# Kernel optimization log

Measured on AMD Instinct MI355X. Metric: run time of the kernel, lower is better.

Reference implementation:

```python
import jax, jax.numpy as jnp
import numpy as np

B, N, ND_, FEAT, WV = 32, 1024, 8, 2048, 300
E, T, STEPS = 20000, 2, 5
NDIM = N * ND_  # 8192


def setup_inputs() -> dict:
    key = jax.random.key(0)
    ks = jax.random.split(key, 20)
    s = 0.02
    inputs = jax.random.normal(ks[0], (B, FEAT), jnp.float32)
    wordvecs = jax.random.normal(ks[1], (N, WV), jnp.float32)
    # unique edges per type (disjoint across types) so the scatter has no duplicate indices
    rng = np.random.default_rng(0)
    codes = rng.permutation(N * N)[: T * E].reshape(T, E)
    edge_u = (codes // N).astype(np.int32)
    edge_v = (codes % N).astype(np.int32)
    ki = np.repeat(np.arange(ND_), ND_)
    kj = np.tile(np.arange(ND_), ND_)
    mat_u = (edge_u.reshape(-1)[:, None] * ND_ + ki[None, :]).reshape(-1).astype(np.int32)
    mat_v = (edge_v.reshape(-1)[:, None] * ND_ + kj[None, :]).reshape(-1).astype(np.int32)
    p = {
        'inputs': inputs, 'wordvecs': wordvecs,
        'edge_u': jnp.asarray(edge_u), 'edge_v': jnp.asarray(edge_v),
        'mat_u': jnp.asarray(mat_u), 'mat_v': jnp.asarray(mat_v),
        # Inputnet: Linear(feat+wv -> 512), Linear(512 -> node_dim)
        'W_in1': jax.random.normal(ks[2], (512, FEAT + WV), jnp.float32) * s,
        'b_in1': jnp.zeros((512,), jnp.float32),
        'W_in2': jax.random.normal(ks[3], (ND_, 512), jnp.float32) * s,
        'b_in2': jnp.zeros((ND_,), jnp.float32),
        # embnet: Linear(wv -> 50)
        'W_emb': jax.random.normal(ks[4], (50, WV), jnp.float32) * s,
        'b_emb': jnp.zeros((50,), jnp.float32),
        # relnets: one (50, 50*nd^2) matrix per edge type
        'rel_mats': jax.random.normal(ks[5], (T, 50, 50 * ND_ * ND_), jnp.float32) * s,
        # GRUCell(node_dim, node_dim)
        'W_ih': jax.random.normal(ks[6], (3 * ND_, ND_), jnp.float32) * s,
        'W_hh': jax.random.normal(ks[7], (3 * ND_, ND_), jnp.float32) * s,
        'b_ih': jnp.zeros((3 * ND_,), jnp.float32),
        'b_hh': jnp.zeros((3 * ND_,), jnp.float32),
        # outnet: Linear(nd -> 20), ReLU, Linear(20 -> 1)
        'W_o1': jax.random.normal(ks[8], (20, ND_), jnp.float32) * s,
        'b_o1': jnp.zeros((20,), jnp.float32),
        'W_o2': jax.random.normal(ks[9], (1, 20), jnp.float32) * s,
        'b_o2': jnp.zeros((1,), jnp.float32),
    }
    return p


def reference(inputs, wordvecs, edge_u, edge_v, mat_u, mat_v,
              W_in1, b_in1, W_in2, b_in2, W_emb, b_emb, rel_mats,
              W_ih, W_hh, b_ih, b_hh, W_o1, b_o1, W_o2, b_o2):
    nd = W_in2.shape[0]
    n_nodes = wordvecs.shape[0]
    ndim = n_nodes * nd
    bsz = inputs.shape[0]

    # Inputnet: per-(image, node) feature -> initial hidden state [B, N*nd]
    f = jnp.concatenate([
        jnp.broadcast_to(inputs[:, None, :], (bsz, n_nodes, inputs.shape[1])),
        jnp.broadcast_to(wordvecs[None, :, :], (bsz, n_nodes, wordvecs.shape[1])),
    ], axis=-1).reshape(bsz * n_nodes, -1)
    h = jax.nn.relu(f @ W_in1.T + b_in1) @ W_in2.T + b_in2  # [B*N, nd]
    hidden = h.reshape(bsz, ndim)

    # edge weights via Relnet per edge type
    embs = wordvecs @ W_emb.T + b_emb  # [N, 50]
    ws = []
    for t in range(rel_mats.shape[0]):
        ue = embs[edge_u[t]]  # [E, 50]
        ve = embs[edge_v[t]]  # [E, 50]
        tmp = (ue @ rel_mats[t]).reshape(ue.shape[0], embs.shape[1], nd * nd)
        ws.append(jnp.einsum('ed,edk->ek', ve, tmp))  # [E, nd^2]
    weights = jnp.concatenate(ws, axis=0).reshape(-1)

    # scatter into dense propagation matrix
    P = jnp.zeros((ndim, ndim), jnp.float32).at[mat_u, mat_v].set(weights)
    norm = jnp.sqrt(jnp.sum(P * P, axis=1))  # row L2 norms [ndim]
    norm = norm + (norm == 0).astype(P.dtype)
    P = P / norm  # NOTE: torch broadcasting divides COLUMNS by row norms (faithful)

    def gru(x, hc):
        gi = x @ W_ih.T + b_ih
        gh = hc @ W_hh.T + b_hh
        ir, iz, inn = jnp.split(gi, 3, axis=-1)
        hr, hz, hn = jnp.split(gh, 3, axis=-1)
        r = jax.nn.sigmoid(ir + hr)
        z = jax.nn.sigmoid(iz + hz)
        n = jnp.tanh(inn + r * hn)
        return (1.0 - z) * n + z * hc

    hiddens = [hidden]
    for _ in range(STEPS):
        x = jnp.tanh(hidden @ P.T)  # [B, ndim]
        hidden = gru(x.reshape(-1, nd), hidden.reshape(-1, nd)).reshape(bsz, ndim)
        hiddens.append(hidden)
    states = jnp.stack(hiddens, axis=1)  # [B, STEPS+1, ndim]

    o = jax.nn.relu(states.reshape(-1, nd) @ W_o1.T + b_o1) @ W_o2.T + b_o2  # [B*(S+1)*N, 1]
    logits = o.reshape(bsz, STEPS + 1, n_nodes).transpose(0, 2, 1)  # [B, N, S+1]
    return logits
```

## Files before the change

### kernel.cpp

```cpp
#include <hip/hip_runtime.h>
#include <math.h>

constexpr int B = 32, N = 1024, ND = 8, FEAT = 2048, WVD = 300;
constexpr int E = 20000, T = 2, STEPS = 5;
constexpr int NDIM = N * ND;
constexpr int H1 = 512;
constexpr int W1C = FEAT + WVD;
constexpr int EMB = 50;
constexpr int RC = EMB * ND * ND;
constexpr int SEG = 16;
constexpr int SEGLEN = E / SEG;
constexpr int KH = 150;

constexpr int G_KA   = 512;
constexpr int G_W1T  = 16 * 10;
constexpr int G_EMB  = N * 25 / 4;
constexpr int G_SEGH = T * N * SEG / 4;
constexpr int F1_TOT = G_KA + G_W1T + G_EMB + G_SEGH;

constexpr int G_ARED = 8;
constexpr int G_WV2  = 512;
constexpr int G_AHAT = 13 * (N / 32) * T;
constexpr int F2_TOT = 1 + G_ARED + G_WV2 + G_AHAT;

constexpr int F4_TOT = 2 * N;

__global__ __launch_bounds__(256) void k_f1(
        const int* eu, int* segcnt,
        const float* inp, const float* W1, float* partA, float* W1T,
        const float* wv, const float* We, const float* be,
        float* embs, float* embsT) {
    __shared__ float smem[8 * 260];
    int tid = threadIdx.x;
    int blk = blockIdx.x;
    if (blk < G_KA) {
        int c = tid & 7, b = tid >> 3;
        int c0 = (blk & 63) * 8;
        int ks = blk >> 6;
        int kt = ks * 256;
        {
            int r = tid >> 5, cb = (tid & 31) * 8;
            const float* src = W1 + (size_t)(c0 + r) * W1C + kt + cb;
            float4 a0 = *(const float4*)src;
            float4 a1 = *(const float4*)(src + 4);
            *(float4*)&smem[r * 260 + cb] = a0;
            *(float4*)&smem[r * 260 + cb + 4] = a1;
        }
        __syncthreads();
        const float* xr = inp + (size_t)b * FEAT + kt;
        float acc = 0.f;
#pragma unroll 8
        for (int k4 = 0; k4 < 64; k4++) {
            float4 x = *(const float4*)(xr + k4 * 4);
            float4 w = *(const float4*)&smem[c * 260 + k4 * 4];
            acc += x.x * w.x + x.y * w.y + x.z * w.z + x.w * w.w;
        }
        partA[(size_t)ks * (H1 * B) + (c0 + c) * B + b] = acc;
    } else if (blk < G_KA + G_W1T) {
        int lb = blk - G_KA;
        int c0 = (lb % 16) * 32, k0 = (lb / 16) * 32;
        float (*tile)[33] = (float(*)[33])smem;
        int kl = tid & 31, cl4 = tid >> 5;
#pragma unroll
        for (int p = 0; p < 4; p++) {
            int c = cl4 + p * 8;
            int k = k0 + kl;
            if (k < WVD) tile[c][kl] = W1[(size_t)(c0 + c) * W1C + FEAT + k];
        }
        __syncthreads();
        int cl = tid & 31, kl4 = tid >> 5;
#pragma unroll
        for (int p = 0; p < 4; p++) {
            int kk = kl4 + p * 8;
            int k = k0 + kk;
            if (k < WVD) W1T[(size_t)k * H1 + c0 + cl] = tile[cl][kk];
        }
    } else if (blk < G_KA + G_W1T + G_EMB) {
        int lb = blk - G_KA - G_W1T;
        int wid = lb * 4 + (tid >> 6);
        int lane = tid & 63;
        int n = wid / 25, cp = wid - n * 25;
        int c0 = cp * 2;
        const float* xr = wv + (size_t)n * WVD;
        const float* wr0 = We + (size_t)c0 * WVD;
        const float* wr1 = wr0 + WVD;
        float a0 = 0.f, a1 = 0.f;
#pragma unroll
        for (int i = 0; i < 5; i++) {
            int k = i * 64 + lane;
            if (k < WVD) {
                float x = xr[k];
                a0 += x * wr0[k];
                a1 += x * wr1[k];
            }
        }
        for (int m = 32; m; m >>= 1) {
            a0 += __shfl_xor(a0, m, 64);
            a1 += __shfl_xor(a1, m, 64);
        }
        if (lane == 0) {
            float v0 = a0 + be[c0], v1 = a1 + be[c0 + 1];
            embs[n * EMB + c0] = v0;
            embs[n * EMB + c0 + 1] = v1;
            embsT[c0 * N + n] = v0;
            embsT[(c0 + 1) * N + n] = v1;
        }
    } else {
        int lb = blk - G_KA - G_W1T - G_EMB;
        int wid = lb * 4 + (tid >> 6);
        int lane = tid & 63;
        int t = wid >> 14, u = (wid >> 4) & (N - 1), seg = wid & (SEG - 1);
        const int* eut = eu + t * E;
        int e0 = seg * SEGLEN, e1 = e0 + SEGLEN, cnt = 0;
        for (int c = e0; c < e1; c += 64) {
            int e = c + lane;
            bool ok = (e < e1) && (eut[e] == u);
            cnt += __popcll(__ballot(ok));
        }
        if (lane == 0) segcnt[wid] = cnt;
    }
}

__global__ __launch_bounds__(256) void k_f2(
        const int* segcnt, int* segoff, int* counts, int* ptr,
        const float* partA, float* AbT,
        const float* wv, const float* W1T, float* Wp,
        const float* embsT, const float* RMbase, float* Ahat) {
    __shared__ float smemf[4096];
    int tid = threadIdx.x, blk = blockIdx.x;
    if (blk == 0) {
        int* sc = (int*)smemf;
        for (int row = tid; row < 2048; row += 256) {
            int acc = 0;
            const int* src = segcnt + row * SEG;
            int* dst = segoff + row * SEG;
#pragma unroll
            for (int s = 0; s < SEG; s++) { dst[s] = acc; acc += src[s]; }
            counts[row] = acc;
            sc[row] = acc;
        }
        __syncthreads();
        int* src = sc; int* dst = sc + 2048;
        for (int st = 1; st < 2048; st <<= 1) {
            for (int j = tid; j < 2048; j += 256)
                dst[j] = src[j] + (j >= st ? src[j - st] : 0);
            __syncthreads();
            int* tmp = src; src = dst; dst = tmp;
        }
        for (int j = tid; j < 2048; j += 256)
            ptr[j] = j ? src[j - 1] : 0;
    } else if (blk <= G_ARED) {
        int cb = (blk - 1) * 2048 + tid * 8;
        if (cb < H1 * B) {
            float4 s0 = {0, 0, 0, 0}, s1 = {0, 0, 0, 0};
#pragma unroll
            for (int ks = 0; ks < 8; ks++) {
                const float* p = partA + (size_t)ks * (H1 * B) + cb;
                float4 a = *(const float4*)p;
                float4 b4 = *(const float4*)(p + 4);
                s0.x += a.x; s0.y += a.y; s0.z += a.z; s0.w += a.w;
                s1.x += b4.x; s1.y += b4.y; s1.z += b4.z; s1.w += b4.w;
            }
            *(float4*)(AbT + cb) = s0;
            *(float4*)(AbT + cb + 4) = s1;
        }
    } else if (blk <= G_ARED + G_WV2) {
        int lb = blk - 1 - G_ARED;
        int kh = lb >> 8;
        int rem = lb & 255;
        int c = (rem & 1) * 256 + tid;
        int n0 = (rem >> 1) * 8;
        int kb = kh * KH;
        float (*el)[152] = (float(*)[152])smemf;
        for (int idx = tid; idx < 8 * KH; idx += 256) {
            int j = idx / KH, k = idx - j * KH;
            el[j][k] = wv[(size_t)(n0 + j) * WVD + kb + k];
        }
        __syncthreads();
        float acc[8] = {};
#pragma unroll 5
        for (int k = 0; k < KH; k++) {
            float r = W1T[(size_t)(kb + k) * H1 + c];
#pragma unroll
            for (int j = 0; j < 8; j++) acc[j] += el[j][k] * r;
        }
        float* wout = Wp + (size_t)kh * N * H1;
#pragma unroll
        for (int j = 0; j < 8; j++) wout[(size_t)(n0 + j) * H1 + c] = acc[j];
    } else {
        int lb = blk - 1 - G_ARED - G_WV2;
        int t = lb / (13 * 32), r = lb % (13 * 32);
        int bx = r % 13, by = r / 13;
        const float* RM = RMbase + (size_t)t * EMB * RC;
        float* Ah = Ahat + (size_t)t * N * RC;
        int n0 = by * 32;
        float (*el)[36] = (float(*)[36])smemf;
        for (int idx = tid; idx < EMB * 32; idx += 256)
            el[idx >> 5][idx & 31] = embsT[(idx >> 5) * N + n0 + (idx & 31)];
        __syncthreads();
        int mi = bx * 256 + (tid & 63) * 4;
        int ni = (tid >> 6) * 8;
        if (mi < RC) {
            float acc[8][4] = {};
#pragma unroll 2
            for (int c = 0; c < EMB; c++) {
                float4 rm = *(const float4*)(RM + (size_t)c * RC + mi);
                float4 e0 = *(const float4*)&el[c][ni];
                float4 e1 = *(const float4*)&el[c][ni + 4];
                float ev[8] = {e0.x, e0.y, e0.z, e0.w, e1.x, e1.y, e1.z, e1.w};
#pragma unroll
                for (int j = 0; j < 8; j++) {
                    acc[j][0] += ev[j] * rm.x;
                    acc[j][1] += ev[j] * rm.y;
                    acc[j][2] += ev[j] * rm.z;
                    acc[j][3] += ev[j] * rm.w;
                }
            }
#pragma unroll
            for (int j = 0; j < 8; j++) {
                float4 o = {acc[j][0], acc[j][1], acc[j][2], acc[j][3]};
                *(float4*)(Ah + (size_t)(n0 + ni + j) * RC + mi) = o;
            }
        }
    }
}

__global__ __launch_bounds__(256) void k_f3(
        const int* eu, const int* ev, const int* ptr, const int* segoff, int* sv) {
    int tid = threadIdx.x, blk = blockIdx.x;
    int wid = blk * 4 + (tid >> 6);
    int lane = tid & 63;
    int t = wid >> 14, u = (wid >> 4) & (N - 1), seg = wid & (SEG - 1);
    const int* eut = eu + t * E;
    const int* evt = ev + t * E;
    int row = t * N + u;
    int base = ptr[row] + segoff[row * SEG + seg];
    int e0 = seg * SEGLEN, e1 = e0 + SEGLEN, cnt = 0;
    for (int c = e0; c < e1; c += 64) {
        int e = c + lane;
        bool ok = (e < e1) && (eut[e] == u);
        unsigned long long m = __ballot(ok);
        if (ok) {
            int rank = __popcll(m & ((1ull << lane) - 1));
            sv[base + cnt + rank] = evt[e];
        }
        cnt += __popcll(m);
    }
}

__global__ __launch_bounds__(256) void k_f4(
        const int* ptr, const int* counts, const int* sv,
        const float* embs, const float* Ahat, float* wbuf, float* inorm,
        const float* AbT, const float* Wp, const float* b1,
        const float* W2, const float* b2, float* sT0) {
    __shared__ float smem[6656];
    int tid = threadIdx.x;
    int blk = blockIdx.x;
    if (blk < N) {
        float* AL = smem;
        int u = blk;
        int wv_ = tid >> 6, k = tid & 63;
        float ssq = 0.f;
        for (int t = 0; t < T; t++) {
            __syncthreads();
            for (int idx = tid; idx < RC; idx += 256)
                AL[idx] = Ahat[((size_t)t * N + u) * RC + idx];
            __syncthreads();
            int base = ptr[t * N + u], cnt = counts[t * N + u];
            for (int i = wv_; i < cnt; i += 4) {
                int slot = base + i;
                int v = sv[slot];
                const float* vr = embs + v * EMB;
                float acc = 0.f;
#pragma unroll 10
                for (int d = 0; d < EMB; d++) acc += vr[d] * AL[d * 64 + k];
                wbuf[(size_t)slot * 64 + k] = acc;
                ssq += acc * acc;
            }
        }
        __syncthreads();
        AL[wv_ * 64 + k] = ssq;
        __syncthreads();
        if (tid < 64) {
            float tot = AL[tid] + AL[64 + tid] + AL[128 + tid] + AL[192 + tid];
            tot += __shfl_xor(tot, 1, 64);
            tot += __shfl_xor(tot, 2, 64);
            tot += __shfl_xor(tot, 4, 64);
            int ki = tid >> 3, kj = tid & 7;
            if (kj == 0) {
                float nv = sqrtf(tot);
                if (nv == 0.f) nv = 1.f;
                inorm[u * ND + ki] = 1.0f / nv;
            }
        }
    } else {
        int n = blk - N;
        float* w2s  = smem;
        float* wvs  = smem + 4096;
        float* part = smem + 4608;
        for (int idx = tid; idx < 8 * H1; idx += 256) w2s[idx] = W2[idx];
        for (int idx = tid; idx < H1; idx += 256)
            wvs[idx] = Wp[(size_t)n * H1 + idx]
                     + Wp[(size_t)N * H1 + (size_t)n * H1 + idx] + b1[idx];
        __syncthreads();
        int b = tid & 31, s = tid >> 5;
        float acc[8] = {};
        for (int i = 0; i < 64; i++) {
            int c = s * 64 + i;
            float tv = fmaxf(AbT[c * 32 + b] + wvs[c], 0.f);
#pragma unroll
            for (int ki = 0; ki < 8; ki++) acc[ki] += tv * w2s[ki * H1 + c];
        }
#pragma unroll
        for (int ki = 0; ki < 8; ki++) part[s * 256 + ki * 32 + b] = acc[ki];
        __syncthreads();
        int ki2 = tid >> 5, b2i = tid & 31;
        float tot = b2[ki2];
#pragma unroll
        for (int s2 = 0; s2 < 8; s2++) tot += part[s2 * 256 + ki2 * 32 + b2i];
        sT0[(size_t)n * 256 + tid] = tot;
    }
}

__global__ __launch_bounds__(256) void k_sc(const int* sv, float* wbuf,
                                            const float* inorm) {
    int idx = blockIdx.x * 256 + threadIdx.x;
    int slot = idx >> 6, k = idx & 63;
    int v = sv[slot];
    wbuf[idx] = wbuf[idx] * inorm[v * ND + (k & 7)];
}

__global__ __launch_bounds__(256) void k_step(
        const int* ptr, const int* counts, const int* sv,
        const float* wbuf, const float* sT, int s,
        const float* W_ih, const float* W_hh, const float* b_ih, const float* b_hh,
        const float* Wo1, const float* bo1, const float* Wo2, const float* bo2,
        float* sOut, float* out, int last) {
    __shared__ float xs[256], hs[256], hfin[256];
    __shared__ float wih[192], whh[192];
    __shared__ float w1s[160], b1s[20], w2s[20];
    __shared__ float res[8][33];
    int tid = threadIdx.x;
    int u = blockIdx.x;
    int ki = tid >> 5, b = tid & 31;
    if (tid < 192) { wih[tid] = W_ih[tid]; whh[tid] = W_hh[tid]; }
    if (last) {
        if (tid < 160) w1s[tid] = Wo1[tid];
        if (tid < 20) { b1s[tid] = bo1[tid]; w2s[tid] = Wo2[tid]; }
    }
    const float* sIn = sT + (size_t)s * NDIM * B;
    float hown = sIn[((size_t)u * 8 + ki) * B + b];
    float acc = 0.f;
    for (int t = 0; t < T; t++) {
        int base = ptr[t * N + u], cnt = counts[t * N + u];
        int i = 0;
        for (; i + 1 < cnt; i += 2) {
            int s0 = base + i, s1 = base + i + 1;
            int v0 = sv[s0], v1 = sv[s1];
            const float* wp0 = wbuf + (size_t)s0 * 64 + ki * 8;
            const float* wp1 = wbuf + (size_t)s1 * 64 + ki * 8;
            float4 wa0 = *(const float4*)wp0;
            float4 wb0 = *(const float4*)(wp0 + 4);
            float4 wa1 = *(const float4*)wp1;
            float4 wb1 = *(const float4*)(wp1 + 4);
            const float* hp0 = sIn + (size_t)v0 * 256 + b;
            const float* hp1 = sIn + (size_t)v1 * 256 + b;
            acc += wa0.x * hp0[0]   + wa0.y * hp0[32]  + wa0.z * hp0[64]  + wa0.w * hp0[96]
                 + wb0.x * hp0[128] + wb0.y * hp0[160] + wb0.z * hp0[192] + wb0.w * hp0[224];
            acc += wa1.x * hp1[0]   + wa1.y * hp1[32]  + wa1.z * hp1[64]  + wa1.w * hp1[96]
                 + wb1.x * hp1[128] + wb1.y * hp1[160] + wb1.z * hp1[192] + wb1.w * hp1[224];
        }
        if (i < cnt) {
            int s0 = base + i;
            int v0 = sv[s0];
            const float* wp0 = wbuf + (size_t)s0 * 64 + ki * 8;
            float4 wa0 = *(const float4*)wp0;
            float4 wb0 = *(const float4*)(wp0 + 4);
            const float* hp0 = sIn + (size_t)v0 * 256 + b;
            acc += wa0.x * hp0[0]   + wa0.y * hp0[32]  + wa0.z * hp0[64]  + wa0.w * hp0[96]
                 + wb0.x * hp0[128] + wb0.y * hp0[160] + wb0.z * hp0[192] + wb0.w * hp0[224];
        }
    }
    float xv = tanhf(acc);
    xs[ki * 32 + b] = xv;
    hs[ki * 32 + b] = hown;
    __syncthreads();
    float gr = b_ih[ki], gz = b_ih[8 + ki], gn = b_ih[16 + ki];
    float hr = b_hh[ki], hz = b_hh[8 + ki], hn = b_hh[16 + ki];
#pragma unroll
    for (int j = 0; j < 8; j++) {
        float xj = xs[j * 32 + b], hj = hs[j * 32 + b];
        gr += wih[ki * 8 + j] * xj;
        gz += wih[(8 + ki) * 8 + j] * xj;
        gn += wih[(16 + ki) * 8 + j] * xj;
        hr += whh[ki * 8 + j] * hj;
        hz += whh[(8 + ki) * 8 + j] * hj;
        hn += whh[(16 + ki) * 8 + j] * hj;
    }
    float r = 1.f / (1.f + expf(-(gr + hr)));
    float z = 1.f / (1.f + expf(-(gz + hz)));
    float nn = tanhf(gn + r * hn);
    float hnew = (1.f - z) * nn + z * hown;
    if (!last) {
        sOut[((size_t)u * 8 + ki) * B + b] = hnew;
        return;
    }
    hfin[ki * 32 + b] = hnew;
    __syncthreads();
    int s6 = tid >> 5, bb = tid & 31;
    if (s6 < 6) {
        float x[8];
#pragma unroll
        for (int kk = 0; kk < 8; kk++)
            x[kk] = (s6 < STEPS)
                ? sT[((size_t)s6 * NDIM + u * 8 + kk) * B + bb]
                : hfin[kk * 32 + bb];
        float accv = bo2[0];
#pragma unroll
        for (int j = 0; j < 20; j++) {
            float h = b1s[j];
#pragma unroll
            for (int kk = 0; kk < 8; kk++) h += w1s[j * 8 + kk] * x[kk];
            h = fmaxf(h, 0.f);
            accv += w2s[j] * h;
        }
        res[s6][bb] = accv;
    }
    __syncthreads();
    if (tid < 192) {
        int b_w = tid / 6, s_w = tid - b_w * 6;
        out[(size_t)b_w * ((STEPS + 1) * N) + u * (STEPS + 1) + s_w] = res[s_w][b_w];
    }
}

extern "C" void kernel_launch(void* const* d_in, const int* in_sizes, int n_in,
                              void* d_out, int out_size, void* d_ws, size_t ws_size,
                              hipStream_t stream) {
    const float* inputs   = (const float*)d_in[0];
    const float* wordvecs = (const float*)d_in[1];
    const int*   edge_u   = (const int*)d_in[2];
    const int*   edge_v   = (const int*)d_in[3];
    const float* W_in1 = (const float*)d_in[6];
    const float* b_in1 = (const float*)d_in[7];
    const float* W_in2 = (const float*)d_in[8];
    const float* b_in2 = (const float*)d_in[9];
    const float* W_emb = (const float*)d_in[10];
    const float* b_emb = (const float*)d_in[11];
    const float* rel_mats = (const float*)d_in[12];
    const float* W_ih = (const float*)d_in[13];
    const float* W_hh = (const float*)d_in[14];
    const float* b_ih = (const float*)d_in[15];
    const float* b_hh = (const float*)d_in[16];
    const float* W_o1 = (const float*)d_in[17];
    const float* b_o1 = (const float*)d_in[18];
    const float* W_o2 = (const float*)d_in[19];
    const float* b_o2 = (const float*)d_in[20];
    float* out = (float*)d_out;

    char* ws = (char*)d_ws;
    size_t off = 0;
    auto alloc = [&](size_t bytes) -> void* {
        void* p = ws + off;
        off = (off + bytes + 255) & ~(size_t)255;
        return p;
    };
    int* segcnt    = (int*)alloc((size_t)T * N * SEG * 4);
    int* segoff    = (int*)alloc((size_t)T * N * SEG * 4);
    int* counts    = (int*)alloc(2048 * 4);
    int* ptr       = (int*)alloc(2048 * 4);
    int* sv        = (int*)alloc((size_t)T * E * 4);
    float* inorm   = (float*)alloc((size_t)NDIM * 4);
    float* partA   = (float*)alloc((size_t)8 * H1 * B * 4);
    float* AbT     = (float*)alloc((size_t)H1 * B * 4);
    float* W1T     = (float*)alloc((size_t)WVD * H1 * 4);
    float* Wp      = (float*)alloc((size_t)2 * N * H1 * 4);
    float* embs    = (float*)alloc((size_t)N * EMB * 4);
    float* embsT   = (float*)alloc((size_t)EMB * N * 4);
    float* Ahat    = (float*)alloc((size_t)T * N * RC * 4);
    float* wbuf    = (float*)alloc((size_t)T * E * 64 * 4);
    float* sT      = (float*)alloc((size_t)(STEPS + 1) * NDIM * B * 4);

    k_f1<<<F1_TOT, 256, 0, stream>>>(edge_u, segcnt, inputs, W_in1, partA, W1T,
                                     wordvecs, W_emb, b_emb, embs, embsT);
    k_f2<<<F2_TOT, 256, 0, stream>>>(segcnt, segoff, counts, ptr,
                                     partA, AbT,
                                     wordvecs, W1T, Wp, embsT, rel_mats, Ahat);
    k_f3<<<T * N * SEG / 4, 256, 0, stream>>>(edge_u, edge_v, ptr, segoff, sv);
    k_f4<<<F4_TOT, 256, 0, stream>>>(ptr, counts, sv, embs, Ahat, wbuf, inorm,
                                     AbT, Wp, b_in1, W_in2, b_in2, sT);
    k_sc<<<T * E * 64 / 256, 256, 0, stream>>>(sv, wbuf, inorm);

    for (int s = 0; s < STEPS; s++) {
        int last = (s == STEPS - 1) ? 1 : 0;
        k_step<<<N, 256, 0, stream>>>(ptr, counts, sv, wbuf, sT, s,
                                      W_ih, W_hh, b_ih, b_hh,
                                      W_o1, b_o1, W_o2, b_o2,
                                      sT + (size_t)(s + 1) * NDIM * B, out, last);
    }
}
```

Measured before the change: 276.0 us.

## Fuse edge bucketing into per-node weight kernel; fold norm scaling into step

Replaces the segmented count, prefix-scan and scatter passes that built a CSR edge list with a per-node scan inside the weight kernel. Each block collects its own node's neighbours through wave ballots into fixed-capacity (64) slots. The separate column-norm rescale kernel is dropped and inorm is applied on the fly inside each propagation step. This cuts three launches and one full pass over wbuf. In exchange, every node block now scans all edges of both types, each step does extra inorm loads, and correctness depends on no node having more than 64 edges per type.

```diff
diff --git a/kernel.cpp b/kernel.cpp
--- a/kernel.cpp
+++ b/kernel.cpp
@@ -8,25 +8,21 @@
 constexpr int W1C = FEAT + WVD;
 constexpr int EMB = 50;
 constexpr int RC = EMB * ND * ND;
-constexpr int SEG = 16;
-constexpr int SEGLEN = E / SEG;
 constexpr int KH = 150;
+constexpr int CAP = 64;
+constexpr int EQ = E / 4;
 
 constexpr int G_KA   = 512;
 constexpr int G_W1T  = 16 * 10;
 constexpr int G_EMB  = N * 25 / 4;
-constexpr int G_SEGH = T * N * SEG / 4;
-constexpr int F1_TOT = G_KA + G_W1T + G_EMB + G_SEGH;
+constexpr int F1_TOT = G_KA + G_W1T + G_EMB;
 
 constexpr int G_ARED = 8;
-constexpr int G_WV2  = 512;
-constexpr int G_AHAT = 13 * (N / 32) * T;
-constexpr int F2_TOT = 1 + G_ARED + G_WV2 + G_AHAT;
-
-constexpr int F4_TOT = 2 * N;
+constexpr int G_WV   = 512;
+constexpr int G_AHAT = 13 * 32 * T;
+constexpr int F2_TOT = G_ARED + G_WV + G_AHAT;
 
 __global__ __launch_bounds__(256) void k_f1(
-        const int* eu, int* segcnt,
         const float* inp, const float* W1, float* partA, float* W1T,
         const float* wv, const float* We, const float* be,
         float* embs, float* embsT) {
@@ -75,7 +71,7 @@
             int k = k0 + kk;
             if (k < WVD) W1T[(size_t)k * H1 + c0 + cl] = tile[cl][kk];
         }
-    } else if (blk < G_KA + G_W1T + G_EMB) {
+    } else {
         int lb = blk - G_KA - G_W1T;
         int wid = lb * 4 + (tid >> 6);
         int lane = tid & 63;
@@ -105,91 +101,58 @@
             embsT[c0 * N + n] = v0;
             embsT[(c0 + 1) * N + n] = v1;
         }
-    } else {
-        int lb = blk - G_KA - G_W1T - G_EMB;
-        int wid = lb * 4 + (tid >> 6);
-        int lane = tid & 63;
-        int t = wid >> 14, u = (wid >> 4) & (N - 1), seg = wid & (SEG - 1);
-        const int* eut = eu + t * E;
-        int e0 = seg * SEGLEN, e1 = e0 + SEGLEN, cnt = 0;
-        for (int c = e0; c < e1; c += 64) {
-            int e = c + lane;
-            bool ok = (e < e1) && (eut[e] == u);
-            cnt += __popcll(__ballot(ok));
-        }
-        if (lane == 0) segcnt[wid] = cnt;
     }
 }
 
 __global__ __launch_bounds__(256) void k_f2(
-        const int* segcnt, int* segoff, int* counts, int* ptr,
         const float* partA, float* AbT,
         const float* wv, const float* W1T, float* Wp,
         const float* embsT, const float* RMbase, float* Ahat) {
-    __shared__ float smemf[4096];
+    __shared__ float smemf[1800];
     int tid = threadIdx.x, blk = blockIdx.x;
-    if (blk == 0) {
-        int* sc = (int*)smemf;
-        for (int row = tid; row < 2048; row += 256) {
-            int acc = 0;
-            const int* src = segcnt + row * SEG;
-            int* dst = segoff + row * SEG;
-#pragma unroll
-            for (int s = 0; s < SEG; s++) { dst[s] = acc; acc += src[s]; }
-            counts[row] = acc;
-            sc[row] = acc;
-        }
-        __syncthreads();
-        int* src = sc; int* dst = sc + 2048;
-        for (int st = 1; st < 2048; st <<= 1) {
-            for (int j = tid; j < 2048; j += 256)
-                dst[j] = src[j] + (j >= st ? src[j - st] : 0);
-            __syncthreads();
-            int* tmp = src; src = dst; dst = tmp;
-        }
-        for (int j = tid; j < 2048; j += 256)
-            ptr[j] = j ? src[j - 1] : 0;
-    } else if (blk <= G_ARED) {
-        int cb = (blk - 1) * 2048 + tid * 8;
-        if (cb < H1 * B) {
-            float4 s0 = {0, 0, 0, 0}, s1 = {0, 0, 0, 0};
-#pragma unroll
-            for (int ks = 0; ks < 8; ks++) {
-                const float* p = partA + (size_t)ks * (H1 * B) + cb;
-                float4 a = *(const float4*)p;
-                float4 b4 = *(const float4*)(p + 4);
-                s0.x += a.x; s0.y += a.y; s0.z += a.z; s0.w += a.w;
-                s1.x += b4.x; s1.y += b4.y; s1.z += b4.z; s1.w += b4.w;
-            }
-            *(float4*)(AbT + cb) = s0;
-            *(float4*)(AbT + cb + 4) = s1;
-        }
-    } else if (blk <= G_ARED + G_WV2) {
-        int lb = blk - 1 - G_ARED;
+    if (blk < G_ARED) {
+        int cb = blk * 2048 + tid * 8;
+        float4 s0 = {0, 0, 0, 0}, s1 = {0, 0, 0, 0};
+#pragma unroll
+        for (int ks = 0; ks < 8; ks++) {
+            const float* p = partA + (size_t)ks * (H1 * B) + cb;
+            float4 a = *(const float4*)p;
+            float4 b4 = *(const float4*)(p + 4);
+            s0.x += a.x; s0.y += a.y; s0.z += a.z; s0.w += a.w;
+            s1.x += b4.x; s1.y += b4.y; s1.z += b4.z; s1.w += b4.w;
+        }
+        *(float4*)(AbT + cb) = s0;
+        *(float4*)(AbT + cb + 4) = s1;
+    } else if (blk < G_ARED + G_WV) {
+        int lb = blk - G_ARED;
         int kh = lb >> 8;
         int rem = lb & 255;
         int c = (rem & 1) * 256 + tid;
         int n0 = (rem >> 1) * 8;
         int kb = kh * KH;
-        float (*el)[152] = (float(*)[152])smemf;
+        float (*el)[8] = (float(*)[8])smemf;
         for (int idx = tid; idx < 8 * KH; idx += 256) {
             int j = idx / KH, k = idx - j * KH;
-            el[j][k] = wv[(size_t)(n0 + j) * WVD + kb + k];
+            el[k][j] = wv[(size_t)(n0 + j) * WVD + kb + k];
         }
         __syncthreads();
         float acc[8] = {};
 #pragma unroll 5
         for (int k = 0; k < KH; k++) {
             float r = W1T[(size_t)(kb + k) * H1 + c];
-#pragma unroll
-            for (int j = 0; j < 8; j++) acc[j] += el[j][k] * r;
+            float4 e0 = *(const float4*)&el[k][0];
+            float4 e1 = *(const float4*)&el[k][4];
+            acc[0] += e0.x * r; acc[1] += e0.y * r;
+            acc[2] += e0.z * r; acc[3] += e0.w * r;
+            acc[4] += e1.x * r; acc[5] += e1.y * r;
+            acc[6] += e1.z * r; acc[7] += e1.w * r;
         }
         float* wout = Wp + (size_t)kh * N * H1;
 #pragma unroll
         for (int j = 0; j < 8; j++) wout[(size_t)(n0 + j) * H1 + c] = acc[j];
     } else {
-        int lb = blk - 1 - G_ARED - G_WV2;
-        int t = lb / (13 * 32), r = lb % (13 * 32);
+        int lb = blk - G_ARED - G_WV;
+        int t = lb / 416, r = lb % 416;
         int bx = r % 13, by = r / 13;
         const float* RM = RMbase + (size_t)t * EMB * RC;
         float* Ah = Ahat + (size_t)t * N * RC;
@@ -226,60 +189,75 @@
 }
 
 __global__ __launch_bounds__(256) void k_f3(
-        const int* eu, const int* ev, const int* ptr, const int* segoff, int* sv) {
-    int tid = threadIdx.x, blk = blockIdx.x;
-    int wid = blk * 4 + (tid >> 6);
-    int lane = tid & 63;
-    int t = wid >> 14, u = (wid >> 4) & (N - 1), seg = wid & (SEG - 1);
-    const int* eut = eu + t * E;
-    const int* evt = ev + t * E;
-    int row = t * N + u;
-    int base = ptr[row] + segoff[row * SEG + seg];
-    int e0 = seg * SEGLEN, e1 = e0 + SEGLEN, cnt = 0;
-    for (int c = e0; c < e1; c += 64) {
-        int e = c + lane;
-        bool ok = (e < e1) && (eut[e] == u);
-        unsigned long long m = __ballot(ok);
-        if (ok) {
-            int rank = __popcll(m & ((1ull << lane) - 1));
-            sv[base + cnt + rank] = evt[e];
-        }
-        cnt += __popcll(m);
-    }
-}
-
-__global__ __launch_bounds__(256) void k_f4(
-        const int* ptr, const int* counts, const int* sv,
+        const int* eu, const int* ev,
         const float* embs, const float* Ahat, float* wbuf, float* inorm,
+        int* counts, int* sv,
         const float* AbT, const float* Wp, const float* b1,
         const float* W2, const float* b2, float* sT0) {
     __shared__ float smem[6656];
+    __shared__ int vl[T][CAP];
+    __shared__ int wcnt[T][4];
     int tid = threadIdx.x;
     int blk = blockIdx.x;
     if (blk < N) {
+        int u = blk;
+        int w = tid >> 6, lane = tid & 63;
+        int* tmpv = (int*)smem;
+        for (int t = 0; t < T; t++) {
+            const int* eut = eu + t * E;
+            const int* evt = ev + t * E;
+            int q0 = w * EQ, q1 = q0 + EQ;
+            int cw = 0;
+            for (int c = q0; c < q1; c += 64) {
+                int e = c + lane;
+                bool ok = (e < q1) && (eut[e] == u);
+                unsigned long long m = __ballot(ok);
+                if (ok) {
+                    int rank = __popcll(m & ((1ull << lane) - 1));
+                    tmpv[(t * 4 + w) * CAP + cw + rank] = evt[e];
+                }
+                cw += __popcll(m);
+            }
+            if (lane == 0) wcnt[t][w] = cw;
+        }
+        __syncthreads();
+        int cnts[T];
+        for (int t = 0; t < T; t++) {
+            int base_w = 0;
+            for (int j = 0; j < w; j++) base_w += wcnt[t][j];
+            int mycnt = wcnt[t][w];
+            int row = t * N + u;
+            for (int i = lane; i < mycnt; i += 64) {
+                int vv = tmpv[(t * 4 + w) * CAP + i];
+                vl[t][base_w + i] = vv;
+                sv[row * CAP + base_w + i] = vv;
+            }
+            cnts[t] = wcnt[t][0] + wcnt[t][1] + wcnt[t][2] + wcnt[t][3];
+            if (tid == 0) counts[row] = cnts[t];
+        }
+        __syncthreads();
         float* AL = smem;
-        int u = blk;
-        int wv_ = tid >> 6, k = tid & 63;
+        int k = lane;
         float ssq = 0.f;
         for (int t = 0; t < T; t++) {
             __syncthreads();
             for (int idx = tid; idx < RC; idx += 256)
                 AL[idx] = Ahat[((size_t)t * N + u) * RC + idx];
             __syncthreads();
-            int base = ptr[t * N + u], cnt = counts[t * N + u];
-            for (int i = wv_; i < cnt; i += 4) {
-                int slot = base + i;
-                int v = sv[slot];
+            int cnt = cnts[t];
+            size_t base = (size_t)(t * N + u) * CAP;
+            for (int i = w; i < cnt; i += 4) {
+                int v = vl[t][i];
                 const float* vr = embs + v * EMB;
                 float acc = 0.f;
 #pragma unroll 10
                 for (int d = 0; d < EMB; d++) acc += vr[d] * AL[d * 64 + k];
-                wbuf[(size_t)slot * 64 + k] = acc;
+                wbuf[(base + i) * 64 + k] = acc;
                 ssq += acc * acc;
             }
         }
         __syncthreads();
-        AL[wv_ * 64 + k] = ssq;
+        AL[w * 64 + k] = ssq;
         __syncthreads();
         if (tid < 64) {
             float tot = AL[tid] + AL[64 + tid] + AL[128 + tid] + AL[192 + tid];
@@ -322,17 +300,9 @@
     }
 }
 
-__global__ __launch_bounds__(256) void k_sc(const int* sv, float* wbuf,
-                                            const float* inorm) {
-    int idx = blockIdx.x * 256 + threadIdx.x;
-    int slot = idx >> 6, k = idx & 63;
-    int v = sv[slot];
-    wbuf[idx] = wbuf[idx] * inorm[v * ND + (k & 7)];
-}
-
 __global__ __launch_bounds__(256) void k_step(
-        const int* ptr, const int* counts, const int* sv,
-        const float* wbuf, const float* sT, int s,
+        const int* counts, const int* sv,
+        const float* wbuf, const float* inorm, const float* sT, int s,
         const float* W_ih, const float* W_hh, const float* b_ih, const float* b_hh,
         const float* Wo1, const float* bo1, const float* Wo2, const float* bo2,
         float* sOut, float* out, int last) {
@@ -352,33 +322,44 @@
     float hown = sIn[((size_t)u * 8 + ki) * B + b];
     float acc = 0.f;
     for (int t = 0; t < T; t++) {
-        int base = ptr[t * N + u], cnt = counts[t * N + u];
+        int row = t * N + u;
+        int cnt = counts[row];
+        size_t base = (size_t)row * CAP;
         int i = 0;
         for (; i + 1 < cnt; i += 2) {
-            int s0 = base + i, s1 = base + i + 1;
+            size_t s0 = base + i, s1 = base + i + 1;
             int v0 = sv[s0], v1 = sv[s1];
-            const float* wp0 = wbuf + (size_t)s0 * 64 + ki * 8;
-            const float* wp1 = wbuf + (size_t)s1 * 64 + ki * 8;
+            const float* wp0 = wbuf + s0 * 64 + ki * 8;
+            const float* wp1 = wbuf + s1 * 64 + ki * 8;
             float4 wa0 = *(const float4*)wp0;
             float4 wb0 = *(const float4*)(wp0 + 4);
             float4 wa1 = *(const float4*)wp1;
             float4 wb1 = *(const float4*)(wp1 + 4);
+            const float* ip0 = inorm + v0 * ND;
+            const float* ip1 = inorm + v1 * ND;
             const float* hp0 = sIn + (size_t)v0 * 256 + b;
             const float* hp1 = sIn + (size_t)v1 * 256 + b;
-            acc += wa0.x * hp0[0]   + wa0.y * hp0[32]  + wa0.z * hp0[64]  + wa0.w * hp0[96]
-                 + wb0.x * hp0[128] + wb0.y * hp0[160] + wb0.z * hp0[192] + wb0.w * hp0[224];
-            acc += wa1.x * hp1[0]   + wa1.y * hp1[32]  + wa1.z * hp1[64]  + wa1.w * hp1[96]
-                 + wb1.x * hp1[128] + wb1.y * hp1[160] + wb1.z * hp1[192] + wb1.w * hp1[224];
+            acc += (wa0.x * ip0[0]) * hp0[0]   + (wa0.y * ip0[1]) * hp0[32]
+                 + (wa0.z * ip0[2]) * hp0[64]  + (wa0.w * ip0[3]) * hp0[96]
+                 + (wb0.x * ip0[4]) * hp0[128] + (wb0.y * ip0[5]) * hp0[160]
+                 + (wb0.z * ip0[6]) * hp0[192] + (wb0.w * ip0[7]) * hp0[224];
+            acc += (wa1.x * ip1[0]) * hp1[0]   + (wa1.y * ip1[1]) * hp1[32]
+                 + (wa1.z * ip1[2]) * hp1[64]  + (wa1.w * ip1[3]) * hp1[96]
+                 + (wb1.x * ip1[4]) * hp1[128] + (wb1.y * ip1[5]) * hp1[160]
+                 + (wb1.z * ip1[6]) * hp1[192] + (wb1.w * ip1[7]) * hp1[224];
         }
         if (i < cnt) {
-            int s0 = base + i;
+            size_t s0 = base + i;
             int v0 = sv[s0];
-            const float* wp0 = wbuf + (size_t)s0 * 64 + ki * 8;
+            const float* wp0 = wbuf + s0 * 64 + ki * 8;
             float4 wa0 = *(const float4*)wp0;
             float4 wb0 = *(const float4*)(wp0 + 4);
+            const float* ip0 = inorm + v0 * ND;
             const float* hp0 = sIn + (size_t)v0 * 256 + b;
-            acc += wa0.x * hp0[0]   + wa0.y * hp0[32]  + wa0.z * hp0[64]  + wa0.w * hp0[96]
-                 + wb0.x * hp0[128] + wb0.y * hp0[160] + wb0.z * hp0[192] + wb0.w * hp0[224];
+            acc += (wa0.x * ip0[0]) * hp0[0]   + (wa0.y * ip0[1]) * hp0[32]
+                 + (wa0.z * ip0[2]) * hp0[64]  + (wa0.w * ip0[3]) * hp0[96]
+                 + (wb0.x * ip0[4]) * hp0[128] + (wb0.y * ip0[5]) * hp0[160]
+                 + (wb0.z * ip0[6]) * hp0[192] + (wb0.w * ip0[7]) * hp0[224];
         }
     }
     float xv = tanhf(acc);
@@ -464,11 +445,8 @@
         off = (off + bytes + 255) & ~(size_t)255;
         return p;
     };
-    int* segcnt    = (int*)alloc((size_t)T * N * SEG * 4);
-    int* segoff    = (int*)alloc((size_t)T * N * SEG * 4);
     int* counts    = (int*)alloc(2048 * 4);
-    int* ptr       = (int*)alloc(2048 * 4);
-    int* sv        = (int*)alloc((size_t)T * E * 4);
+    int* sv        = (int*)alloc((size_t)T * N * CAP * 4);
     float* inorm   = (float*)alloc((size_t)NDIM * 4);
     float* partA   = (float*)alloc((size_t)8 * H1 * B * 4);
     float* AbT     = (float*)alloc((size_t)H1 * B * 4);
@@ -477,22 +455,19 @@
     float* embs    = (float*)alloc((size_t)N * EMB * 4);
     float* embsT   = (float*)alloc((size_t)EMB * N * 4);
     float* Ahat    = (float*)alloc((size_t)T * N * RC * 4);
-    float* wbuf    = (float*)alloc((size_t)T * E * 64 * 4);
+    float* wbuf    = (float*)alloc((size_t)T * N * CAP * 64 * 4);
     float* sT      = (float*)alloc((size_t)(STEPS + 1) * NDIM * B * 4);
 
-    k_f1<<<F1_TOT, 256, 0, stream>>>(edge_u, segcnt, inputs, W_in1, partA, W1T,
+    k_f1<<<F1_TOT, 256, 0, stream>>>(inputs, W_in1, partA, W1T,
                                      wordvecs, W_emb, b_emb, embs, embsT);
-    k_f2<<<F2_TOT, 256, 0, stream>>>(segcnt, segoff, counts, ptr,
-                                     partA, AbT,
-                                     wordvecs, W1T, Wp, embsT, rel_mats, Ahat);
-    k_f3<<<T * N * SEG / 4, 256, 0, stream>>>(edge_u, edge_v, ptr, segoff, sv);
-    k_f4<<<F4_TOT, 256, 0, stream>>>(ptr, counts, sv, embs, Ahat, wbuf, inorm,
-                                     AbT, Wp, b_in1, W_in2, b_in2, sT);
-    k_sc<<<T * E * 64 / 256, 256, 0, stream>>>(sv, wbuf, inorm);
+    k_f2<<<F2_TOT, 256, 0, stream>>>(partA, AbT, wordvecs, W1T, Wp,
+                                     embsT, rel_mats, Ahat);
+    k_f3<<<2 * N, 256, 0, stream>>>(edge_u, edge_v, embs, Ahat, wbuf, inorm,
+                                    counts, sv, AbT, Wp, b_in1, W_in2, b_in2, sT);
 
     for (int s = 0; s < STEPS; s++) {
         int last = (s == STEPS - 1) ? 1 : 0;
-        k_step<<<N, 256, 0, stream>>>(ptr, counts, sv, wbuf, sT, s,
+        k_step<<<N, 256, 0, stream>>>(counts, sv, wbuf, inorm, sT, s,
                                       W_ih, W_hh, b_ih, b_hh,
                                       W_o1, b_o1, W_o2, b_o2,
                                       sT + (size_t)(s + 1) * NDIM * B, out, last);
```

After: 252.8 us. 8.4% less time.
